# Kernel optimization log

Hardware: AMD Instinct MI355X
Metric: run time of the kernel (lower is better)

## Reference

```python
import jax, jax.numpy as jnp
import numpy as np

D_MODEL = 1024
NUM_HEADS = 16
HEAD_DIM = D_MODEL // NUM_HEADS
B, L = 4, 4096


def _linear(x, w, b):
    # torch nn.Linear: y = x @ w.T + b, w: [out, in]
    return jnp.einsum('bld,od->blo', x, w) + b


def _elu_feature_map(x):
    return jax.nn.elu(x) + 1.0


def setup_inputs() -> dict:
    key = jax.random.key(0)
    ks = jax.random.split(key, 11)
    s = 1.0 / np.sqrt(D_MODEL)
    inp = {
        'query': jax.random.normal(ks[0], (B, L, D_MODEL), jnp.float32),
        'key': jax.random.normal(ks[1], (B, L, D_MODEL), jnp.float32),
        'value': jax.random.normal(ks[2], (B, L, D_MODEL), jnp.float32),
        'wq': jax.random.uniform(ks[3], (D_MODEL, D_MODEL), jnp.float32, -s, s),
        'bq': jax.random.uniform(ks[4], (D_MODEL,), jnp.float32, -s, s),
        'wk': jax.random.uniform(ks[5], (D_MODEL, D_MODEL), jnp.float32, -s, s),
        'bk': jax.random.uniform(ks[6], (D_MODEL,), jnp.float32, -s, s),
        'wv': jax.random.uniform(ks[7], (D_MODEL, D_MODEL), jnp.float32, -s, s),
        'bv': jax.random.uniform(ks[8], (D_MODEL,), jnp.float32, -s, s),
        'wo': jax.random.uniform(ks[9], (D_MODEL, D_MODEL), jnp.float32, -s, s),
        'bo': jax.random.uniform(ks[10], (D_MODEL,), jnp.float32, -s, s),
    }
    return inp


def reference(query, key, value, wq, bq, wk, bk, wv, bv, wo, bo):
    Bsz, Lq, _ = query.shape
    # project and split heads -> [B, H, L, hd]
    def split_heads(x):
        return x.reshape(Bsz, -1, NUM_HEADS, HEAD_DIM).transpose(0, 2, 1, 3)
    Q = split_heads(_linear(query, wq, bq))
    K = split_heads(_linear(key, wk, bk))
    V = split_heads(_linear(value, wv, bv))
    Q = _elu_feature_map(Q)
    K = _elu_feature_map(K)
    # KV: [B, H, hd, hd]
    KV = jnp.einsum('bhld,bhle->bhde', K, V)
    Ksum = K.sum(axis=2)  # [B, H, hd]
    Z = 1.0 / (jnp.einsum('bhld,bhd->bhl', Q, Ksum) + 1e-6)  # [B, H, Lq]
    out = jnp.einsum('bhld,bhde->bhle', Q, KV) * Z[..., None]
    out = out.transpose(0, 2, 1, 3).reshape(Bsz, Lq, D_MODEL)
    return _linear(out, wo, bo)
```

## Files before the change

### kernel.cpp

```cpp
#include <hip/hip_runtime.h>
#include <hip/hip_bf16.h>

typedef _Float16 half8 __attribute__((ext_vector_type(8)));
typedef _Float16 half4 __attribute__((ext_vector_type(4)));
typedef float f32x4 __attribute__((ext_vector_type(4)));

#define KDIM 1024
#define NDIM 1024
#define MROWS 16384

#define GLD_LDS16(g, l)                                                  \
  __builtin_amdgcn_global_load_lds(                                      \
      (const __attribute__((address_space(1))) void*)(g),                \
      (__attribute__((address_space(3))) void*)(l), 16, 0, 0)

__global__ __launch_bounds__(256)
void cvt_f32_to_f16(const float* __restrict__ src, _Float16* __restrict__ dst,
                    int n8) {
  for (int i = blockIdx.x * 256 + threadIdx.x; i < n8; i += gridDim.x * 256) {
    float4 f0 = ((const float4*)src)[2 * i];
    float4 f1 = ((const float4*)src)[2 * i + 1];
    half8 h;
    h[0] = (_Float16)f0.x; h[1] = (_Float16)f0.y;
    h[2] = (_Float16)f0.z; h[3] = (_Float16)f0.w;
    h[4] = (_Float16)f1.x; h[5] = (_Float16)f1.y;
    h[6] = (_Float16)f1.z; h[7] = (_Float16)f1.w;
    ((half8*)dst)[i] = h;
  }
}

template <int ACT, int TRANS, int FUSE, typename TOUT>
__global__ __launch_bounds__(512, 2)
void gemm_big(const _Float16* __restrict__ X, const _Float16* __restrict__ W,
              const float* __restrict__ bias, TOUT* __restrict__ Y,
              const _Float16* __restrict__ KVTx) {
  constexpr int BM = 256, BN = 128, BK = 64;
  __shared__ _Float16 As[3 * BM * BK];
  __shared__ _Float16 Bs[3 * BN * BK];

  const int tid  = threadIdx.x;
  const int lane = tid & 63;
  const int w    = tid >> 6;
  const int wm   = w >> 1;
  const int wn   = w & 1;

  const int bid = blockIdx.x;
  const int wid = (bid & 7) * 64 + (bid >> 3);
  const int m0  = (wid >> 3) * BM;
  const int n0  = (wid & 7) * BN;

  const int lr = lane >> 3;
  const int ls = (lane & 7) ^ lr;

#define STAGE_TILE(kt, bidx)                                                  \
  {                                                                           \
    const int k0s = (kt) * BK;                                                \
    _Float16* la = As + (bidx) * (BM * BK) + w * 512;                         \
    _Float16* lb = Bs + (bidx) * (BN * BK) + w * 512;                         \
    _Pragma("unroll")                                                         \
    for (int j = 0; j < 4; ++j)                                               \
      GLD_LDS16(X + (size_t)(m0 + w * 8 + 64 * j + lr) * KDIM + k0s + ls * 8, \
                la + 4096 * j);                                               \
    _Pragma("unroll")                                                         \
    for (int j = 0; j < 2; ++j)                                               \
      GLD_LDS16(W + (size_t)(n0 + w * 8 + 64 * j + lr) * KDIM + k0s + ls * 8, \
                lb + 4096 * j);                                               \
  }

  f32x4 acc[4][4] = {};

  STAGE_TILE(0, 0);
  STAGE_TILE(1, 1);
  asm volatile("s_waitcnt vmcnt(6)" ::: "memory");
  asm volatile("s_barrier" ::: "memory");

  int bc = 0;
  for (int t = 0; t < 16; ++t) {
    int bs = bc + 2; if (bs >= 3) bs -= 3;
    const char* Ab = (const char*)As + bc * (BM * BK * 2);
    const char* Bb = (const char*)Bs + bc * (BN * BK * 2);

    half8 afr[4][2], bfr[4][2];
#pragma unroll
    for (int mi = 0; mi < 4; ++mi)
#pragma unroll
      for (int kk = 0; kk < 2; ++kk) {
        int row  = wm * 64 + mi * 16 + (lane & 15);
        int byte = row * 128 + ((lane >> 4) << 4) + kk * 64;
        byte ^= (row & 7) << 4;
        afr[mi][kk] = *(const half8*)(Ab + byte);
      }
#pragma unroll
    for (int ni = 0; ni < 4; ++ni)
#pragma unroll
      for (int kk = 0; kk < 2; ++kk) {
        int row  = wn * 64 + ni * 16 + (lane & 15);
        int byte = row * 128 + ((lane >> 4) << 4) + kk * 64;
        byte ^= (row & 7) << 4;
        bfr[ni][kk] = *(const half8*)(Bb + byte);
      }

    if (t < 14) STAGE_TILE(t + 2, bs);

    __builtin_amdgcn_s_setprio(1);
#pragma unroll
    for (int kk = 0; kk < 2; ++kk)
#pragma unroll
      for (int mi = 0; mi < 4; ++mi)
#pragma unroll
        for (int ni = 0; ni < 4; ++ni)
          acc[mi][ni] = __builtin_amdgcn_mfma_f32_16x16x32_f16(
              afr[mi][kk], bfr[ni][kk], acc[mi][ni], 0, 0, 0);
    __builtin_amdgcn_s_setprio(0);

    if (t < 14) {
      asm volatile("s_waitcnt vmcnt(6)" ::: "memory");
      asm volatile("s_barrier" ::: "memory");
    } else if (t == 14) {
      asm volatile("s_waitcnt vmcnt(0)" ::: "memory");
      asm volatile("s_barrier" ::: "memory");
    }
    ++bc; if (bc == 3) bc = 0;
  }
#undef STAGE_TILE

  if constexpr (FUSE) {
    __syncthreads();
    _Float16* Ct = As;
#pragma unroll
    for (int ni = 0; ni < 4; ++ni) {
      int cl   = wn * 64 + ni * 16 + (lane & 15);
      float bv = bias[n0 + cl];
#pragma unroll
      for (int mi = 0; mi < 4; ++mi) {
#pragma unroll
        for (int i = 0; i < 4; ++i) {
          int row = wm * 64 + mi * 16 + ((lane >> 4) << 2) + i;
          float v = acc[mi][ni][i] + bv;
          v = (v > 0.f) ? (v + 1.f) : __expf(v);
          int byte = row * 256 + cl * 2;
          byte ^= (row & 7) << 4;
          *(_Float16*)((char*)Ct + byte) = (_Float16)v;
        }
      }
    }
    _Float16* KVs = Bs;
    const int bh0 = ((m0 >> 12) << 4) + (n0 >> 6);
    for (int c = tid; c < 1280; c += 512) {
      int hh  = (c >= 640) ? 1 : 0;
      int cc  = c - hh * 640;
      int row = cc >> 3;
      int co8 = (cc & 7) << 3;
      int byte = hh * 10240 + row * 128 + co8 * 2;
      byte ^= (row & 7) << 4;
      *(half8*)((char*)KVs + byte) =
          *(const half8*)(KVTx + (size_t)(bh0 + hh) * 5120 + cc * 8);
    }
    __syncthreads();
    f32x4 acc2[4][5] = {};
#pragma unroll
    for (int kk = 0; kk < 2; ++kk) {
      half8 afr2[4], bfr2[5];
#pragma unroll
      for (int m = 0; m < 4; ++m) {
        int row  = wm * 64 + m * 16 + (lane & 15);
        int byte = row * 256 + wn * 128 + kk * 64 + ((lane >> 4) << 4);
        byte ^= (row & 7) << 4;
        afr2[m] = *(const half8*)((const char*)Ct + byte);
      }
#pragma unroll
      for (int n = 0; n < 5; ++n) {
        int row  = n * 16 + (lane & 15);
        int byte = wn * 10240 + row * 128 + kk * 64 + ((lane >> 4) << 4);
        byte ^= (row & 7) << 4;
        bfr2[n] = *(const half8*)((const char*)KVs + byte);
      }
#pragma unroll
      for (int m = 0; m < 4; ++m)
#pragma unroll
        for (int n = 0; n < 5; ++n)
          acc2[m][n] = __builtin_amdgcn_mfma_f32_16x16x32_f16(
              afr2[m], bfr2[n], acc2[m][n], 0, 0, 0);
    }
#pragma unroll
    for (int m = 0; m < 4; ++m) {
#pragma unroll
      for (int i = 0; i < 4; ++i) {
        float dn = __shfl(acc2[m][4][i], lane & 48);
        float z  = 1.f / (dn + 1e-6f);
        size_t row = (size_t)m0 + wm * 64 + m * 16 + ((lane >> 4) << 2) + i;
#pragma unroll
        for (int n = 0; n < 4; ++n) {
          int col = n0 + wn * 64 + n * 16 + (lane & 15);
          Y[row * NDIM + col] = (TOUT)(acc2[m][n][i] * z);
        }
      }
    }
    return;
  }

#pragma unroll
  for (int ni = 0; ni < 4; ++ni) {
    int col  = n0 + wn * 64 + ni * 16 + (lane & 15);
    float bv = bias[col];
#pragma unroll
    for (int mi = 0; mi < 4; ++mi) {
      int r0 = m0 + wm * 64 + mi * 16 + ((lane >> 4) << 2);
      if constexpr (TRANS) {
        int b  = r0 >> 12;
        int l0 = r0 & 4095;
        half4 hv;
#pragma unroll
        for (int i = 0; i < 4; ++i) {
          float v = acc[mi][ni][i] + bv;
          if constexpr (ACT == 1) v = (v > 0.f) ? (v + 1.f) : __expf(v);
          hv[i] = (_Float16)v;
        }
        *(half4*)((_Float16*)Y + ((size_t)(b * 1024 + col)) * 4096 + l0) = hv;
      } else {
#pragma unroll
        for (int i = 0; i < 4; ++i) {
          float v = acc[mi][ni][i] + bv;
          if constexpr (ACT == 1) v = (v > 0.f) ? (v + 1.f) : __expf(v);
          Y[(size_t)(r0 + i) * NDIM + col] = (TOUT)v;
        }
      }
    }
  }
}

__global__ __launch_bounds__(256, 2)
void kv_mfma(const _Float16* __restrict__ KT, const _Float16* __restrict__ VT,
             _Float16* __restrict__ pKV) {
  const int bh = blockIdx.x;
  const int ch = blockIdx.y;
  const int tid  = threadIdx.x;
  const int lane = tid & 63;
  const int w    = tid >> 6;

  __shared__ _Float16 As[64 * 64];
  __shared__ _Float16 Bs[64 * 64];

  const int lr = lane >> 3;
  const int ls = (lane & 7) ^ lr;
  const size_t lbase = (size_t)ch * 512 + ls * 8;
  const _Float16* gA = VT + (size_t)(bh * 64 + w * 16 + lr) * 4096 + lbase;
  const _Float16* gB = KT + (size_t)(bh * 64 + w * 16 + lr) * 4096 + lbase;
  _Float16* ldsA = As + (w * 16) * 64;
  _Float16* ldsB = Bs + (w * 16) * 64;

  half8 aones;
#pragma unroll
  for (int j = 0; j < 8; ++j) aones[j] = (lane & 15) == 0 ? (_Float16)1.0f : (_Float16)0.0f;

  f32x4 acc[5] = {};

  for (int k0 = 0; k0 < 512; k0 += 64) {
    __syncthreads();
#pragma unroll
    for (int c = 0; c < 2; ++c) {
      GLD_LDS16(gA + k0 + (size_t)(c * 8) * 4096, ldsA + c * 8 * 64);
      GLD_LDS16(gB + k0 + (size_t)(c * 8) * 4096, ldsB + c * 8 * 64);
    }
    __syncthreads();

    half8 afr[4][2], bfr[2];
#pragma unroll
    for (int m = 0; m < 4; ++m)
#pragma unroll
      for (int kk = 0; kk < 2; ++kk) {
        int row  = m * 16 + (lane & 15);
        int byte = row * 128 + ((lane >> 4) << 4) + kk * 64;
        byte ^= (row & 7) << 4;
        afr[m][kk] = *(const half8*)((const char*)As + byte);
      }
#pragma unroll
    for (int kk = 0; kk < 2; ++kk) {
      int row  = w * 16 + (lane & 15);
      int byte = row * 128 + ((lane >> 4) << 4) + kk * 64;
      byte ^= (row & 7) << 4;
      bfr[kk] = *(const half8*)((const char*)Bs + byte);
    }
#pragma unroll
    for (int kk = 0; kk < 2; ++kk) {
#pragma unroll
      for (int m = 0; m < 4; ++m)
        acc[m] = __builtin_amdgcn_mfma_f32_16x16x32_f16(afr[m][kk], bfr[kk],
                                                        acc[m], 0, 0, 0);
      acc[4] = __builtin_amdgcn_mfma_f32_16x16x32_f16(aones, bfr[kk],
                                                      acc[4], 0, 0, 0);
    }
  }

  _Float16* outp = pKV + ((size_t)ch * 64 + bh) * 5120;
  const int col = w * 16 + (lane & 15);
#pragma unroll
  for (int m = 0; m < 5; ++m) {
#pragma unroll
    for (int i = 0; i < 4; ++i) {
      int row = m * 16 + ((lane >> 4) << 2) + i;
      outp[row * 64 + col] = (_Float16)acc[m][i];
    }
  }
}

__global__ __launch_bounds__(256)
void kv_combine(const _Float16* __restrict__ pKV, _Float16* __restrict__ KVTx) {
  int g = blockIdx.x * 256 + threadIdx.x;
  int bh = g / 5120;
  int j  = g - bh * 5120;
  float s = 0.f;
#pragma unroll
  for (int ch = 0; ch < 8; ++ch)
    s += (float)pKV[((size_t)ch * 64 + bh) * 5120 + j];
  KVTx[(size_t)bh * 5120 + j] = (_Float16)s;
}

extern "C" void kernel_launch(void* const* d_in, const int* in_sizes, int n_in,
                              void* d_out, int out_size, void* d_ws, size_t ws_size,
                              hipStream_t stream) {
  const float* q  = (const float*)d_in[0];
  const float* k  = (const float*)d_in[1];
  const float* v  = (const float*)d_in[2];
  const float* wq = (const float*)d_in[3];
  const float* bq = (const float*)d_in[4];
  const float* wk = (const float*)d_in[5];
  const float* bk = (const float*)d_in[6];
  const float* wv = (const float*)d_in[7];
  const float* bv = (const float*)d_in[8];
  const float* wo = (const float*)d_in[9];
  const float* bo = (const float*)d_in[10];
  float* out = (float*)d_out;

  char* ws = (char*)d_ws;
  _Float16* KT   = (_Float16*)(ws + 33554432);
  _Float16* VT   = (_Float16*)(ws + 67108864);
  _Float16* Wh   = (_Float16*)(ws + 100663296);
  _Float16* pKVh = (_Float16*)(ws + 102760448);
  _Float16* KVTx = (_Float16*)(ws + 108003328);
  _Float16* att  = KT;
  _Float16* Xh   = (_Float16*)d_out;

  const int N8_BIG = MROWS * KDIM / 8;
  const int N8_W   = KDIM * KDIM / 8;

  const int GBLK = (MROWS / 256) * (NDIM / 128);

  cvt_f32_to_f16<<<2048, 256, 0, stream>>>(k, Xh, N8_BIG);
  cvt_f32_to_f16<<<512, 256, 0, stream>>>(wk, Wh, N8_W);
  gemm_big<1, 1, 0, _Float16><<<GBLK, 512, 0, stream>>>(Xh, Wh, bk, KT, nullptr);
  cvt_f32_to_f16<<<2048, 256, 0, stream>>>(v, Xh, N8_BIG);
  cvt_f32_to_f16<<<512, 256, 0, stream>>>(wv, Wh, N8_W);
  gemm_big<0, 1, 0, _Float16><<<GBLK, 512, 0, stream>>>(Xh, Wh, bv, VT, nullptr);

  kv_mfma<<<dim3(64, 8), 256, 0, stream>>>(KT, VT, pKVh);
  kv_combine<<<1280, 256, 0, stream>>>(pKVh, KVTx);

  cvt_f32_to_f16<<<2048, 256, 0, stream>>>(q, Xh, N8_BIG);
  cvt_f32_to_f16<<<512, 256, 0, stream>>>(wq, Wh, N8_W);
  gemm_big<1, 0, 1, _Float16><<<GBLK, 512, 0, stream>>>(Xh, Wh, bq, att, KVTx);

  cvt_f32_to_f16<<<512, 256, 0, stream>>>(wo, Wh, N8_W);
  gemm_big<0, 0, 0, float><<<GBLK, 512, 0, stream>>>(att, Wh, bo, out, nullptr);
}
```

Before: 263.8 us.

## Batch conversions, add triple-buffered BK32 GEMM for K/V, halve KV split

Batches the f32-to-f16 conversions of the three weights and the three activations into two multi-buffer launches, with the buffers rearranged across workspace and output memory. Adds a new K/V projection GEMM with BK=32, a three-stage LDS ring buffer, manual waitcnt/barrier scheduling, setprio around the MFMAs and higher occupancy. Also halves the number of K-split chunks in the KV reduction (1024 rows each instead of 512) and shortens the combine loop to match. These changes aim to cut launch count and hide global-load latency, but they add aliasing risk across buffers and give the KV kernel less parallelism.

```diff
diff --git a/kernel.cpp b/kernel.cpp
--- a/kernel.cpp
+++ b/kernel.cpp
@@ -17,6 +17,25 @@
 __global__ __launch_bounds__(256)
 void cvt_f32_to_f16(const float* __restrict__ src, _Float16* __restrict__ dst,
                     int n8) {
+  for (int i = blockIdx.x * 256 + threadIdx.x; i < n8; i += gridDim.x * 256) {
+    float4 f0 = ((const float4*)src)[2 * i];
+    float4 f1 = ((const float4*)src)[2 * i + 1];
+    half8 h;
+    h[0] = (_Float16)f0.x; h[1] = (_Float16)f0.y;
+    h[2] = (_Float16)f0.z; h[3] = (_Float16)f0.w;
+    h[4] = (_Float16)f1.x; h[5] = (_Float16)f1.y;
+    h[6] = (_Float16)f1.z; h[7] = (_Float16)f1.w;
+    ((half8*)dst)[i] = h;
+  }
+}
+
+__global__ __launch_bounds__(256)
+void cvt_multi3(const float* __restrict__ s0, _Float16* __restrict__ d0,
+                const float* __restrict__ s1, _Float16* __restrict__ d1,
+                const float* __restrict__ s2, _Float16* __restrict__ d2,
+                int n8) {
+  const float* src = (blockIdx.y == 0) ? s0 : (blockIdx.y == 1) ? s1 : s2;
+  _Float16*    dst = (blockIdx.y == 0) ? d0 : (blockIdx.y == 1) ? d1 : d2;
   for (int i = blockIdx.x * 256 + threadIdx.x; i < n8; i += gridDim.x * 256) {
     float4 f0 = ((const float4*)src)[2 * i];
     float4 f1 = ((const float4*)src)[2 * i + 1];
@@ -229,6 +248,119 @@
   }
 }
 
+template <int ACT, int TRANS, typename TOUT>
+__global__ __launch_bounds__(512, 4)
+void gemm_bk32(const _Float16* __restrict__ X, const _Float16* __restrict__ W,
+               const float* __restrict__ bias, TOUT* __restrict__ Y) {
+  constexpr int BM = 256, BN = 128, BK = 32;
+  __shared__ _Float16 As[3 * BM * BK];
+  __shared__ _Float16 Bs[3 * BN * BK];
+
+  const int tid  = threadIdx.x;
+  const int lane = tid & 63;
+  const int w    = tid >> 6;
+  const int wm   = w >> 1;
+  const int wn   = w & 1;
+
+  const int bid = blockIdx.x;
+  const int wid = (bid & 7) * 64 + (bid >> 3);
+  const int m0  = (wid >> 3) * BM;
+  const int n0  = (wid & 7) * BN;
+
+  const int lrw = lane >> 2;
+  const int gsl = (lane & 3) ^ (lrw & 3);
+  const _Float16* gA = X + (size_t)(m0 + w * 16 + lrw) * KDIM + gsl * 8;
+  const _Float16* gB = W + (size_t)(n0 + w * 16 + lrw) * KDIM + gsl * 8;
+
+#define STAGE32(kt, bidx)                                                     \
+  {                                                                           \
+    const int k0s = (kt) * BK;                                                \
+    _Float16* la = As + (bidx) * (BM * BK) + (w * 16) * BK;                   \
+    _Float16* lb = Bs + (bidx) * (BN * BK) + (w * 16) * BK;                   \
+    GLD_LDS16(gA + k0s, la);                                                  \
+    GLD_LDS16(gA + (size_t)128 * KDIM + k0s, la + 128 * BK);                  \
+    GLD_LDS16(gB + k0s, lb);                                                  \
+  }
+
+  const int rsl = ((lane >> 4) ^ (lane & 3)) << 4;
+
+  f32x4 acc[4][4] = {};
+
+  STAGE32(0, 0);
+  STAGE32(1, 1);
+  asm volatile("s_waitcnt vmcnt(3)" ::: "memory");
+  asm volatile("s_barrier" ::: "memory");
+
+  int bc = 0;
+  for (int t = 0; t < 32; ++t) {
+    int bs = bc + 2; if (bs >= 3) bs -= 3;
+    const char* Ab = (const char*)As + bc * (BM * BK * 2);
+    const char* Bb = (const char*)Bs + bc * (BN * BK * 2);
+
+    half8 afr[4], bfr[4];
+#pragma unroll
+    for (int mi = 0; mi < 4; ++mi) {
+      int row = wm * 64 + mi * 16 + (lane & 15);
+      afr[mi] = *(const half8*)(Ab + row * 64 + rsl);
+    }
+#pragma unroll
+    for (int ni = 0; ni < 4; ++ni) {
+      int row = wn * 64 + ni * 16 + (lane & 15);
+      bfr[ni] = *(const half8*)(Bb + row * 64 + rsl);
+    }
+
+    if (t < 30) STAGE32(t + 2, bs);
+
+    __builtin_amdgcn_s_setprio(1);
+#pragma unroll
+    for (int mi = 0; mi < 4; ++mi)
+#pragma unroll
+      for (int ni = 0; ni < 4; ++ni)
+        acc[mi][ni] = __builtin_amdgcn_mfma_f32_16x16x32_f16(
+            afr[mi], bfr[ni], acc[mi][ni], 0, 0, 0);
+    __builtin_amdgcn_s_setprio(0);
+
+    if (t < 30) {
+      asm volatile("s_waitcnt vmcnt(3)" ::: "memory");
+      asm volatile("s_barrier" ::: "memory");
+    } else if (t == 30) {
+      asm volatile("s_waitcnt vmcnt(0)" ::: "memory");
+      asm volatile("s_barrier" ::: "memory");
+    }
+    ++bc; if (bc == 3) bc = 0;
+  }
+#undef STAGE32
+
+#pragma unroll
+  for (int ni = 0; ni < 4; ++ni) {
+    int col  = n0 + wn * 64 + ni * 16 + (lane & 15);
+    float bv = bias[col];
+#pragma unroll
+    for (int mi = 0; mi < 4; ++mi) {
+      int r0 = m0 + wm * 64 + mi * 16 + ((lane >> 4) << 2);
+      if constexpr (TRANS) {
+        int b  = r0 >> 12;
+        int l0 = r0 & 4095;
+        half4 hv;
+#pragma unroll
+        for (int i = 0; i < 4; ++i) {
+          float v = acc[mi][ni][i] + bv;
+          if constexpr (ACT == 1) v = (v > 0.f) ? (v + 1.f) : __expf(v);
+          hv[i] = (_Float16)v;
+        }
+        *(half4*)((_Float16*)Y + ((size_t)(b * 1024 + col)) * 4096 + l0) = hv;
+      } else {
+#pragma unroll
+        for (int i = 0; i < 4; ++i) {
+          float v = acc[mi][ni][i] + bv;
+          if constexpr (ACT == 1) v = (v > 0.f) ? (v + 1.f) : __expf(v);
+          Y[(size_t)(r0 + i) * NDIM + col] = (TOUT)v;
+        }
+      }
+    }
+  }
+}
+
 __global__ __launch_bounds__(256, 2)
 void kv_mfma(const _Float16* __restrict__ KT, const _Float16* __restrict__ VT,
              _Float16* __restrict__ pKV) {
@@ -243,7 +375,7 @@
 
   const int lr = lane >> 3;
   const int ls = (lane & 7) ^ lr;
-  const size_t lbase = (size_t)ch * 512 + ls * 8;
+  const size_t lbase = (size_t)ch * 1024 + ls * 8;
   const _Float16* gA = VT + (size_t)(bh * 64 + w * 16 + lr) * 4096 + lbase;
   const _Float16* gB = KT + (size_t)(bh * 64 + w * 16 + lr) * 4096 + lbase;
   _Float16* ldsA = As + (w * 16) * 64;
@@ -255,7 +387,7 @@
 
   f32x4 acc[5] = {};
 
-  for (int k0 = 0; k0 < 512; k0 += 64) {
+  for (int k0 = 0; k0 < 1024; k0 += 64) {
     __syncthreads();
 #pragma unroll
     for (int c = 0; c < 2; ++c) {
@@ -311,7 +443,7 @@
   int j  = g - bh * 5120;
   float s = 0.f;
 #pragma unroll
-  for (int ch = 0; ch < 8; ++ch)
+  for (int ch = 0; ch < 4; ++ch)
     s += (float)pKV[((size_t)ch * 64 + bh) * 5120 + j];
   KVTx[(size_t)bh * 5120 + j] = (_Float16)s;
 }
@@ -333,33 +465,36 @@
   float* out = (float*)d_out;
 
   char* ws = (char*)d_ws;
+  _Float16* Xq   = (_Float16*)(ws);
   _Float16* KT   = (_Float16*)(ws + 33554432);
   _Float16* VT   = (_Float16*)(ws + 67108864);
-  _Float16* Wh   = (_Float16*)(ws + 100663296);
-  _Float16* pKVh = (_Float16*)(ws + 102760448);
-  _Float16* KVTx = (_Float16*)(ws + 108003328);
+  _Float16* whk  = (_Float16*)(ws + 100663296);
+  _Float16* whv  = (_Float16*)(ws + 102760448);
+  _Float16* whq  = (_Float16*)(ws + 104857600);
+  _Float16* pKV  = (_Float16*)(ws + 100663296);
+  _Float16* who  = (_Float16*)(ws + 100663296);
   _Float16* att  = KT;
-  _Float16* Xh   = (_Float16*)d_out;
+  _Float16* Xk   = (_Float16*)d_out;
+  _Float16* Xv   = (_Float16*)((char*)d_out + 33554432);
+  _Float16* KVTx = (_Float16*)((char*)d_out + 33554432);
 
   const int N8_BIG = MROWS * KDIM / 8;
   const int N8_W   = KDIM * KDIM / 8;
 
   const int GBLK = (MROWS / 256) * (NDIM / 128);
 
-  cvt_f32_to_f16<<<2048, 256, 0, stream>>>(k, Xh, N8_BIG);
-  cvt_f32_to_f16<<<512, 256, 0, stream>>>(wk, Wh, N8_W);
-  gemm_big<1, 1, 0, _Float16><<<GBLK, 512, 0, stream>>>(Xh, Wh, bk, KT, nullptr);
-  cvt_f32_to_f16<<<2048, 256, 0, stream>>>(v, Xh, N8_BIG);
-  cvt_f32_to_f16<<<512, 256, 0, stream>>>(wv, Wh, N8_W);
-  gemm_big<0, 1, 0, _Float16><<<GBLK, 512, 0, stream>>>(Xh, Wh, bv, VT, nullptr);
-
-  kv_mfma<<<dim3(64, 8), 256, 0, stream>>>(KT, VT, pKVh);
-  kv_combine<<<1280, 256, 0, stream>>>(pKVh, KVTx);
-
-  cvt_f32_to_f16<<<2048, 256, 0, stream>>>(q, Xh, N8_BIG);
-  cvt_f32_to_f16<<<512, 256, 0, stream>>>(wq, Wh, N8_W);
-  gemm_big<1, 0, 1, _Float16><<<GBLK, 512, 0, stream>>>(Xh, Wh, bq, att, KVTx);
-
-  cvt_f32_to_f16<<<512, 256, 0, stream>>>(wo, Wh, N8_W);
-  gemm_big<0, 0, 0, float><<<GBLK, 512, 0, stream>>>(att, Wh, bo, out, nullptr);
-}
+  cvt_multi3<<<dim3(512, 3), 256, 0, stream>>>(wq, whq, wk, whk, wv, whv, N8_W);
+  cvt_multi3<<<dim3(2048, 3), 256, 0, stream>>>(k, Xk, v, Xv, q, Xq, N8_BIG);
+
+  gemm_bk32<1, 1, _Float16><<<GBLK, 512, 0, stream>>>(Xk, whk, bk, KT);
+  gemm_bk32<0, 1, _Float16><<<GBLK, 512, 0, stream>>>(Xv, whv, bv, VT);
+
+  kv_mfma<<<dim3(64, 4), 256, 0, stream>>>(KT, VT, pKV);
+  kv_combine<<<1280, 256, 0, stream>>>(pKV, KVTx);
+
+  cvt_f32_to_f16<<<512, 256, 0, stream>>>(wo, who, N8_W);
+
+  gemm_big<1, 0, 1, _Float16><<<GBLK, 512, 0, stream>>>(Xq, whq, bq, att, KVTx);
+
+  gemm_big<0, 0, 0, float><<<GBLK, 512, 0, stream>>>(att, who, bo, out, nullptr);
+}
```

Measured after the change: 252.3 us. 4.4% less time.
